# Kernel tuning notes

Hardware: AMD Instinct MI355X
Metric: run time of the kernel (lower is better)

The kernel has to match this reference:

```python
import jax, jax.numpy as jnp
import numpy as np

EPS = 1e-08

def rotate_half(x):
    # split last dim into 2 halves: '... (j d) -> ... j d', j=2
    x1, x2 = jnp.split(x, 2, axis=-1)
    return jnp.concatenate((-x2, x1), axis=-1)

def apply_rotary_pos_emb(t, freqs):
    seq_len = t.shape[-2]
    freqs = freqs[:, :, -seq_len:]
    return t * jnp.cos(freqs) + rotate_half(t) * jnp.sin(freqs)

def setup_inputs() -> dict:
    key = jax.random.key(0)
    ks = jax.random.split(key, 6)
    B, N, D, H, DH = 2, 2048, 1024, 16, 64
    inner = H * DH
    x = jax.random.normal(ks[0], (B, N, D), dtype=jnp.float32)
    # realistic rotary frequencies over dim_head
    inv_freq = 1.0 / (10000.0 ** (np.arange(0, DH, 2, dtype=np.float32) / DH))
    t = np.arange(N, dtype=np.float32)
    freqs = np.einsum('n,f->nf', t, inv_freq)            # [N, DH/2]
    pos_emb = jnp.asarray(np.concatenate([freqs, freqs], axis=-1)[None, None])  # [1,1,N,DH]
    gamma = jnp.ones((D,), dtype=jnp.float32)
    Wq = jax.random.normal(ks[1], (D, inner), dtype=jnp.float32) * (D ** -0.5)
    Wkv = jax.random.normal(ks[2], (D, 2 * inner), dtype=jnp.float32) * (D ** -0.5)
    Wo = jax.random.normal(ks[3], (inner, D), dtype=jnp.float32) * (inner ** -0.5)
    bo = jnp.zeros((D,), dtype=jnp.float32)
    return {"x": x, "pos_emb": pos_emb, "gamma": gamma, "Wq": Wq, "Wkv": Wkv, "Wo": Wo, "bo": bo}

def reference(x, pos_emb, gamma, Wq, Wkv, Wo, bo):
    B, N, D = x.shape
    H = 16
    DH = Wq.shape[1] // H
    scale = DH ** -0.5
    # NOTE: kv_input is the UN-normalized x (captured before RMSNorm in the original)
    kv_input = x
    # RMSNorm: x / clamp(||x|| * dim^-0.5, eps) * gamma
    norm = jnp.linalg.norm(x, axis=-1, keepdims=True) * (D ** -0.5)
    xn = x / jnp.maximum(norm, EPS) * gamma
    q = xn @ Wq                                   # [B,N,H*DH]
    kv = kv_input @ Wkv
    k, v = jnp.split(kv, 2, axis=-1)
    def to_heads(t):
        return t.reshape(B, N, H, DH).transpose(0, 2, 1, 3)  # b h n d
    q, k, v = to_heads(q), to_heads(k), to_heads(v)
    q = q * scale
    q = apply_rotary_pos_emb(q, pos_emb)
    k = apply_rotary_pos_emb(k, pos_emb)
    sim = jnp.einsum('bhid,bhjd->bhij', q, k)
    i, j = sim.shape[-2:]
    causal_mask = jnp.triu(jnp.ones((i, j), dtype=bool), k=j - i + 1)
    mask_value = -jnp.finfo(sim.dtype).max
    sim = jnp.where(causal_mask, mask_value, sim)
    attn = jax.nn.softmax(sim, axis=-1)
    out = jnp.einsum('bhij,bhjd->bhid', attn, v)
    out = out.transpose(0, 2, 1, 3).reshape(B, N, H * DH)
    return out @ Wo + bo
```

## Files before the change

### kernel.cpp

```cpp
#include <hip/hip_runtime.h>
#include <cmath>

#define B_ 2
#define N_ 2048
#define D_ 1024
#define H_ 16

typedef __attribute__((ext_vector_type(8))) short short8;
typedef __attribute__((ext_vector_type(4))) float f32x4;
typedef __attribute__((ext_vector_type(4))) unsigned short u16x4;

__device__ __forceinline__ unsigned short f2bf(float f) {
    union { float f; unsigned u; } x;
    x.f = f;
    unsigned r = x.u + 0x7FFFu + ((x.u >> 16) & 1u);
    return (unsigned short)(r >> 16);
}
__device__ __forceinline__ float bf2f(unsigned short u) {
    union { unsigned u; float f; } x;
    x.u = ((unsigned)u) << 16;
    return x.f;
}
__device__ __forceinline__ unsigned cvt_pk_bf16(float lo, float hi) {
    unsigned r;
    asm("v_cvt_pk_bf16_f32 %0, %1, %2" : "=v"(r) : "v"(lo), "v"(hi));
    return r;
}
__device__ __forceinline__ float exp2_fast(float x) {
    float r;
    asm("v_exp_f32 %0, %1" : "=v"(r) : "v"(x));
    return r;
}
__device__ __forceinline__ void gload_lds16(const void* g, void* l) {
    __builtin_amdgcn_global_load_lds((const __attribute__((address_space(1))) unsigned*)g,
                                     (__attribute__((address_space(3))) unsigned*)l,
                                     16, 0, 0);
}

__global__ __launch_bounds__(256) void freqtab_kernel(const float* __restrict__ pos,
                                                      float2* __restrict__ tabq,
                                                      float2* __restrict__ tabk) {
    const int idx = blockIdx.x * 256 + threadIdx.x;
    const float f = pos[idx];
    const float cc = cosf(f), ss = sinf(f);
    const float sq = 0.125f * 1.4426950408889634f;
    tabq[idx] = make_float2(sq * cc, sq * ss);
    tabk[idx] = make_float2(cc, ss);
}

__global__ __launch_bounds__(256) void rmsnorm_kernel(const float* __restrict__ x,
                                                      unsigned short* __restrict__ xb,
                                                      float* __restrict__ s) {
    const int row = blockIdx.x;
    const float4 v = reinterpret_cast<const float4*>(x + (size_t)row * D_)[threadIdx.x];
    float ss = v.x * v.x + v.y * v.y + v.z * v.z + v.w * v.w;
    #pragma unroll
    for (int off = 32; off; off >>= 1) ss += __shfl_xor(ss, off, 64);
    __shared__ float wss[4];
    if ((threadIdx.x & 63) == 0) wss[threadIdx.x >> 6] = ss;
    __syncthreads();
    const float tot = wss[0] + wss[1] + wss[2] + wss[3];
    const float inv = 1.0f / fmaxf(sqrtf(tot * (1.0f / D_)), 1e-8f);
    if (threadIdx.x == 0) s[row] = inv;
    u16x4 ox;
    ox[0] = f2bf(v.x); ox[1] = f2bf(v.y); ox[2] = f2bf(v.z); ox[3] = f2bf(v.w);
    *reinterpret_cast<u16x4*>(xb + (size_t)row * D_ + threadIdx.x * 4) = ox;
}

__global__ __launch_bounds__(256) void convT_all_kernel(const float* __restrict__ Wq,
                                                        const float* __restrict__ Wkv,
                                                        const float* __restrict__ Wo,
                                                        const float* __restrict__ gamma,
                                                        unsigned short* __restrict__ Wqt,
                                                        unsigned short* __restrict__ Wkvt,
                                                        unsigned short* __restrict__ Wot) {
    __shared__ float tile[32][33];
    const int bx = blockIdx.x;
    const float* W;
    unsigned short* Wt;
    int Nm, n0;
    bool gmul = false;
    if (bx < 32)       { W = Wq;  Wt = Wqt;  Nm = 1024; n0 = bx * 32; gmul = true; }
    else if (bx < 96)  { W = Wkv; Wt = Wkvt; Nm = 2048; n0 = (bx - 32) * 32; }
    else               { W = Wo;  Wt = Wot;  Nm = 1024; n0 = (bx - 96) * 32; }
    const int k0 = blockIdx.y * 32;
    const int r = threadIdx.x >> 3, c4 = (threadIdx.x & 7) * 4;
    const float4 ld = *reinterpret_cast<const float4*>(W + (size_t)(k0 + r) * Nm + n0 + c4);
    tile[r][c4 + 0] = ld.x; tile[r][c4 + 1] = ld.y;
    tile[r][c4 + 2] = ld.z; tile[r][c4 + 3] = ld.w;
    __syncthreads();
    u16x4 o;
    #pragma unroll
    for (int j = 0; j < 4; ++j) {
        float v = tile[c4 + j][r];
        if (gmul) v *= gamma[k0 + c4 + j];
        o[j] = f2bf(v);
    }
    *reinterpret_cast<u16x4*>(Wt + (size_t)(n0 + r) * 1024 + k0 + c4) = o;
}

__global__ __launch_bounds__(256) void gemm_qkv_kernel(const unsigned short* __restrict__ xb,
                                                       const unsigned short* __restrict__ Wqt,
                                                       const unsigned short* __restrict__ Wkvt,
                                                       const float* __restrict__ s,
                                                       unsigned short* __restrict__ qb,
                                                       unsigned short* __restrict__ kb,
                                                       unsigned short* __restrict__ vt,
                                                       const float2* __restrict__ tabq,
                                                       const float2* __restrict__ tabk) {
    __shared__ unsigned short As[2][64 * 64];
    __shared__ unsigned short Bs[2][128 * 64];
    __shared__ float sld[64];
    const int bid = blockIdx.x;
    const int xcd = bid & 7;
    const int ii = bid >> 3;
    const int bx = xcd * 3 + (ii % 3);
    const int m0 = (ii / 3) * 64;

    const unsigned short* Bt;
    int n0;
    if (bx < 8)       { Bt = Wqt;  n0 = bx * 128; }
    else if (bx < 16) { Bt = Wkvt; n0 = (bx - 8) * 128; }
    else              { Bt = Wkvt; n0 = (bx - 16) * 128 + 1024; }

    const int tid = threadIdx.x, lane = tid & 63, w = tid >> 6;
    const int wm = w >> 1, wn = w & 1;
    const int cc = lane & 15;
    const int sr = tid >> 3;
    const int sc = (tid & 7) * 8;

    if (tid < 64) sld[tid] = s[m0 + tid];

    f32x4 acc[2][4] = {};

    #pragma unroll
    for (int i = 0; i < 4; ++i) {
        const int r = i * 32 + sr;
        const int cs = sc ^ ((r & 7) << 3);
        if (i < 2)
            gload_lds16(xb + (size_t)(m0 + r) * 1024 + cs, (char*)As[0] + i * 4096 + w * 1024);
        gload_lds16(Bt + (size_t)(n0 + r) * 1024 + cs, (char*)Bs[0] + i * 4096 + w * 1024);
    }

    for (int t = 0; t < 16; ++t) {
        if (t + 1 < 16) {
            const int k0 = (t + 1) * 64;
            char* ad = (char*)As[(t + 1) & 1];
            char* bd = (char*)Bs[(t + 1) & 1];
            #pragma unroll
            for (int i = 0; i < 4; ++i) {
                const int r = i * 32 + sr;
                const int cs = sc ^ ((r & 7) << 3);
                if (i < 2)
                    gload_lds16(xb + (size_t)(m0 + r) * 1024 + k0 + cs, ad + i * 4096 + w * 1024);
                gload_lds16(Bt + (size_t)(n0 + r) * 1024 + k0 + cs, bd + i * 4096 + w * 1024);
            }
            asm volatile("s_waitcnt vmcnt(6)" ::: "memory");
        } else {
            asm volatile("s_waitcnt vmcnt(0)" ::: "memory");
        }
        __builtin_amdgcn_s_barrier();

        const char* Ac = (const char*)As[t & 1];
        const char* Bc = (const char*)Bs[t & 1];

        short8 af[2][2], bf[4][2];
        #pragma unroll
        for (int mf = 0; mf < 2; ++mf)
            #pragma unroll
            for (int ks = 0; ks < 2; ++ks) {
                const int r = wm * 32 + mf * 16 + cc;
                const int cb = (ks * 64 + ((lane >> 4) * 16)) ^ ((r & 7) << 4);
                af[mf][ks] = *reinterpret_cast<const short8*>(Ac + r * 128 + cb);
            }
        #pragma unroll
        for (int nf = 0; nf < 4; ++nf)
            #pragma unroll
            for (int ks = 0; ks < 2; ++ks) {
                const int r = wn * 64 + nf * 16 + cc;
                const int cb = (ks * 64 + ((lane >> 4) * 16)) ^ ((r & 7) << 4);
                bf[nf][ks] = *reinterpret_cast<const short8*>(Bc + r * 128 + cb);
            }
        #pragma unroll
        for (int ks = 0; ks < 2; ++ks)
            #pragma unroll
            for (int mf = 0; mf < 2; ++mf)
                #pragma unroll
                for (int nf = 0; nf < 4; ++nf)
                    acc[mf][nf] = __builtin_amdgcn_mfma_f32_16x16x32_bf16(af[mf][ks], bf[nf][ks], acc[mf][nf], 0, 0, 0);

        __builtin_amdgcn_s_barrier();
    }

    if (bx < 16) {
        const float2* tab = (bx < 8) ? tabq : tabk;
        unsigned short* dst = (bx < 8) ? qb : kb;
        const bool doscale = (bx < 8);
        #pragma unroll
        for (int mf = 0; mf < 2; ++mf)
            #pragma unroll
            for (int reg = 0; reg < 4; ++reg) {
                const int rloc = wm * 32 + mf * 16 + (lane >> 4) * 4 + reg;
                const int row = m0 + rloc;
                const int n = row & (N_ - 1);
                const float srow = doscale ? sld[rloc] : 1.0f;
                #pragma unroll
                for (int nf = 0; nf < 2; ++nf) {
                    const int d = nf * 16 + cc;
                    const float2 t1 = tab[n * 64 + d];
                    const float2 t2 = tab[n * 64 + 32 + d];
                    const float x1 = acc[mf][nf][reg] * srow;
                    const float x2 = acc[mf][nf + 2][reg] * srow;
                    const float o1 = x1 * t1.x - x2 * t1.y;
                    const float o2 = x2 * t2.x + x1 * t2.y;
                    const int col = n0 + wn * 64 + nf * 16 + cc;
                    dst[(size_t)row * 1024 + col] = f2bf(o1);
                    dst[(size_t)row * 1024 + col + 32] = f2bf(o2);
                }
            }
    } else {
        const int bb = m0 >> 11;
        const int nbase = (m0 & (N_ - 1)) + wm * 32;
        #pragma unroll
        for (int mf = 0; mf < 2; ++mf) {
            const int nloc = nbase + mf * 16 + (lane >> 4) * 4;
            #pragma unroll
            for (int nf = 0; nf < 4; ++nf) {
                const int cv = n0 - 1024 + wn * 64 + nf * 16 + cc;
                const int h = cv >> 6, d = cv & 63;
                uint2 u;
                u.x = cvt_pk_bf16(acc[mf][nf][0], acc[mf][nf][1]);
                u.y = cvt_pk_bf16(acc[mf][nf][2], acc[mf][nf][3]);
                *reinterpret_cast<uint2*>(vt + ((size_t)(bb * 16 + h) * 64 + d) * 2048 + nloc) = u;
            }
        }
    }
}

__global__ __launch_bounds__(256) void gemm_o_kernel(const unsigned short* __restrict__ A,
                                                     const unsigned short* __restrict__ Bt,
                                                     const float* __restrict__ bias,
                                                     float* __restrict__ Cout) {
    __shared__ unsigned short As[2][128 * 64];
    __shared__ unsigned short Bs[2][64 * 64];
    const int bid = blockIdx.x;
    const int xcd = bid & 7;
    const int ii = bid >> 3;
    const int n0 = (xcd * 2 + (ii & 1)) * 64;
    const int m0 = (ii >> 1) * 128;
    const int tid = threadIdx.x, lane = tid & 63, w = tid >> 6;
    const int wm = w >> 1, wn = w & 1;
    const int cc = lane & 15;
    const int sr = tid >> 3;
    const int sc = (tid & 7) * 8;

    f32x4 acc[4][2] = {};

    #pragma unroll
    for (int i = 0; i < 4; ++i) {
        const int r = i * 32 + sr;
        const int cs = sc ^ ((r & 7) << 3);
        gload_lds16(A + (size_t)(m0 + r) * 1024 + cs, (char*)As[0] + i * 4096 + w * 1024);
        if (i < 2)
            gload_lds16(Bt + (size_t)(n0 + r) * 1024 + cs, (char*)Bs[0] + i * 4096 + w * 1024);
    }

    for (int t = 0; t < 16; ++t) {
        if (t + 1 < 16) {
            const int k0 = (t + 1) * 64;
            char* ad = (char*)As[(t + 1) & 1];
            char* bd = (char*)Bs[(t + 1) & 1];
            #pragma unroll
            for (int i = 0; i < 4; ++i) {
                const int r = i * 32 + sr;
                const int cs = sc ^ ((r & 7) << 3);
                gload_lds16(A + (size_t)(m0 + r) * 1024 + k0 + cs, ad + i * 4096 + w * 1024);
                if (i < 2)
                    gload_lds16(Bt + (size_t)(n0 + r) * 1024 + k0 + cs, bd + i * 4096 + w * 1024);
            }
            asm volatile("s_waitcnt vmcnt(6)" ::: "memory");
        } else {
            asm volatile("s_waitcnt vmcnt(0)" ::: "memory");
        }
        __builtin_amdgcn_s_barrier();

        const char* Ac = (const char*)As[t & 1];
        const char* Bc = (const char*)Bs[t & 1];

        short8 af[4][2], bf[2][2];
        #pragma unroll
        for (int mf = 0; mf < 4; ++mf)
            #pragma unroll
            for (int ks = 0; ks < 2; ++ks) {
                const int r = wm * 64 + mf * 16 + cc;
                const int cb = (ks * 64 + ((lane >> 4) * 16)) ^ ((r & 7) << 4);
                af[mf][ks] = *reinterpret_cast<const short8*>(Ac + r * 128 + cb);
            }
        #pragma unroll
        for (int nf = 0; nf < 2; ++nf)
            #pragma unroll
            for (int ks = 0; ks < 2; ++ks) {
                const int r = wn * 32 + nf * 16 + cc;
                const int cb = (ks * 64 + ((lane >> 4) * 16)) ^ ((r & 7) << 4);
                bf[nf][ks] = *reinterpret_cast<const short8*>(Bc + r * 128 + cb);
            }
        #pragma unroll
        for (int ks = 0; ks < 2; ++ks)
            #pragma unroll
            for (int mf = 0; mf < 4; ++mf)
                #pragma unroll
                for (int nf = 0; nf < 2; ++nf)
                    acc[mf][nf] = __builtin_amdgcn_mfma_f32_16x16x32_bf16(af[mf][ks], bf[nf][ks], acc[mf][nf], 0, 0, 0);

        __builtin_amdgcn_s_barrier();
    }

    float bb[2];
    #pragma unroll
    for (int nf = 0; nf < 2; ++nf) bb[nf] = bias[n0 + wn * 32 + nf * 16 + cc];
    #pragma unroll
    for (int mf = 0; mf < 4; ++mf)
        #pragma unroll
        for (int nf = 0; nf < 2; ++nf)
            #pragma unroll
            for (int reg = 0; reg < 4; ++reg) {
                const int row = m0 + wm * 64 + mf * 16 + (lane >> 4) * 4 + reg;
                const int col = n0 + wn * 32 + nf * 16 + cc;
                Cout[(size_t)row * 1024 + col] = acc[mf][nf][reg] + bb[nf];
            }
}

__global__ __launch_bounds__(256, 5) void attn_mfma_kernel(const unsigned short* __restrict__ q,
                                                           const unsigned short* __restrict__ kb,
                                                           const unsigned short* __restrict__ vt,
                                                           unsigned short* __restrict__ att,
                                                           unsigned short* __restrict__ pO,
                                                           float2* __restrict__ pml) {
    const int bid = blockIdx.x;
    const int xcd = bid & 7;
    const int rest = bid >> 3;
    const int bh = xcd * 4 + rest / 48;
    const int s = 47 - (rest % 48);
    int qi, t0, t1, half;
    bool split;
    if (s < 16) {
        qi = s; t0 = 0; t1 = qi + 1; half = 0; split = false;
    } else {
        const int qs = s - 16;
        qi = 16 + (qs >> 1);
        half = qs & 1;
        const int hmid = (qi + 2) >> 1;
        t0 = half ? hmid : 0;
        t1 = half ? (qi + 1) : hmid;
        split = true;
    }
    const int b = bh >> 4, h = bh & 15;
    const int qb_ = qi * 64;
    const int tid = threadIdx.x;
    const int lane = tid & 63;
    const int w = tid >> 6;
    const int c = lane & 15;
    const int g = lane >> 4;

    __shared__ __align__(16) unsigned short Ks[2][64 * 64];
    __shared__ __align__(16) unsigned short Vs[64 * 64];
    __shared__ __align__(16) unsigned short Ps[4][1024];
    char* const PB = (char*)&Ps[w][0];

    const int qrow = qb_ + w * 16 + c;
    short8 qf[2];
    {
        const unsigned short* qp = q + (size_t)(b * N_ + qrow) * 1024 + h * 64 + g * 8;
        qf[0] = *reinterpret_cast<const short8*>(qp);
        qf[1] = *reinterpret_cast<const short8*>(qp + 32);
    }

    float m = -1e30f, l = 0.f;
    f32x4 oacc[4] = {};

    const int sr = tid >> 3, sc = (tid & 7) * 8;
    const unsigned short* kbase = kb + (size_t)b * N_ * 1024 + h * 64;
    const unsigned short* vbase = vt + (size_t)bh * 64 * 2048;

    #pragma unroll
    for (int i = 0; i < 2; ++i) {
        const int r = i * 32 + sr;
        const int cs = sc ^ ((r & 7) << 3);
        gload_lds16(kbase + (size_t)(t0 * 64 + r) * 1024 + cs,
                    (char*)Ks[t0 & 1] + i * 4096 + w * 1024);
        gload_lds16(vbase + (size_t)r * 2048 + t0 * 64 + cs,
                    (char*)Vs + i * 4096 + w * 1024);
    }

    for (int t = t0; t < t1; ++t) {
        const int jb = t * 64;
        const int jn = jb + 64;
        if (t + 1 < t1) {
            char* kd = (char*)Ks[(t + 1) & 1];
            #pragma unroll
            for (int i = 0; i < 2; ++i) {
                const int r = i * 32 + sr;
                const int cs = sc ^ ((r & 7) << 3);
                gload_lds16(kbase + (size_t)(jn + r) * 1024 + cs, kd + i * 4096 + w * 1024);
            }
            asm volatile("s_waitcnt vmcnt(2)" ::: "memory");
        } else {
            asm volatile("s_waitcnt vmcnt(0)" ::: "memory");
        }
        __builtin_amdgcn_s_barrier();

        const char* Ksc = (const char*)Ks[t & 1];
        const char* Vsc = (const char*)Vs;

        f32x4 st[4];
        __builtin_amdgcn_s_setprio(1);
        #pragma unroll
        for (int ct = 0; ct < 4; ++ct) {
            const int key = ct * 16 + c;
            f32x4 acc = {0.f, 0.f, 0.f, 0.f};
            #pragma unroll
            for (int ks = 0; ks < 2; ++ks) {
                const int addr = (key * 128 + ks * 64 + g * 16) ^ ((key & 7) << 4);
                const short8 kf = *reinterpret_cast<const short8*>(Ksc + addr);
                acc = __builtin_amdgcn_mfma_f32_16x16x32_bf16(kf, qf[ks], acc, 0, 0, 0);
            }
            st[ct] = acc;
        }
        __builtin_amdgcn_s_setprio(0);

        float mx = -1e30f;
        if (jb + 63 > qrow) {
            #pragma unroll
            for (int ct = 0; ct < 4; ++ct)
                #pragma unroll
                for (int reg = 0; reg < 4; ++reg) {
                    const int key = jb + ct * 16 + g * 4 + reg;
                    const float sv = (key <= qrow) ? st[ct][reg] : -1e30f;
                    st[ct][reg] = sv;
                    mx = fmaxf(mx, sv);
                }
        } else {
            #pragma unroll
            for (int ct = 0; ct < 4; ++ct)
                mx = fmaxf(mx, fmaxf(fmaxf(st[ct][0], st[ct][1]),
                                     fmaxf(st[ct][2], st[ct][3])));
        }
        mx = fmaxf(mx, __shfl_xor(mx, 16, 64));
        mx = fmaxf(mx, __shfl_xor(mx, 32, 64));
        if (!__all(mx <= m + 8.0f)) {
            const float mn = fmaxf(m, mx);
            const float corr = exp2_fast(m - mn);
            l *= corr;
            m = mn;
            #pragma unroll
            for (int dt = 0; dt < 4; ++dt) {
                oacc[dt][0] *= corr; oacc[dt][1] *= corr;
                oacc[dt][2] *= corr; oacc[dt][3] *= corr;
            }
        }
        float rs = 0.f;
        #pragma unroll
        for (int ct = 0; ct < 4; ++ct)
            #pragma unroll
            for (int reg = 0; reg < 4; ++reg) {
                const float p = exp2_fast(st[ct][reg] - m);
                st[ct][reg] = p;
                rs += p;
            }
        rs += __shfl_xor(rs, 16, 64);
        rs += __shfl_xor(rs, 32, 64);
        l += rs;

        #pragma unroll
        for (int ct = 0; ct < 4; ++ct) {
            uint2 u;
            u.x = cvt_pk_bf16(st[ct][0], st[ct][1]);
            u.y = cvt_pk_bf16(st[ct][2], st[ct][3]);
            const int addr = (c * 128 + ct * 32 + g * 8) ^ ((c & 7) << 4);
            *reinterpret_cast<uint2*>(PB + addr) = u;
        }
        short8 pf[2];
        #pragma unroll
        for (int ks = 0; ks < 2; ++ks) {
            const int addr = (c * 128 + ks * 64 + g * 16) ^ ((c & 7) << 4);
            pf[ks] = *reinterpret_cast<const short8*>(PB + addr);
        }
        __builtin_amdgcn_s_setprio(1);
        #pragma unroll
        for (int dt = 0; dt < 4; ++dt) {
            #pragma unroll
            for (int ks = 0; ks < 2; ++ks) {
                const int vd = dt * 16 + c;
                const int addr = (vd * 128 + ks * 64 + g * 16) ^ ((vd & 7) << 4);
                const short8 vf = *reinterpret_cast<const short8*>(Vsc + addr);
                oacc[dt] = __builtin_amdgcn_mfma_f32_16x16x32_bf16(vf, pf[ks], oacc[dt], 0, 0, 0);
            }
        }
        __builtin_amdgcn_s_setprio(0);

        __builtin_amdgcn_s_barrier();

        if (t + 1 < t1) {
            #pragma unroll
            for (int i = 0; i < 2; ++i) {
                const int r = i * 32 + sr;
                const int cs = sc ^ ((r & 7) << 3);
                gload_lds16(vbase + (size_t)r * 2048 + jn + cs, (char*)Vs + i * 4096 + w * 1024);
            }
        }
    }

    if (!split) {
        const float inv = 1.0f / l;
        unsigned short* orow = att + (size_t)(b * N_ + qrow) * 1024 + h * 64;
        #pragma unroll
        for (int dt = 0; dt < 4; ++dt) {
            #pragma unroll
            for (int rp = 0; rp < 2; ++rp) {
                const unsigned u = cvt_pk_bf16(oacc[dt][2 * rp] * inv,
                                               oacc[dt][2 * rp + 1] * inv);
                *reinterpret_cast<unsigned*>(orow + dt * 16 + g * 4 + rp * 2) = u;
            }
        }
    } else {
        const int slot = (bh * 16 + (qi - 16)) * 2 + half;
        const int rloc = w * 16 + c;
        pml[slot * 64 + rloc] = make_float2(m, l);
        unsigned short* prow = pO + (size_t)slot * 4096 + rloc * 64;
        #pragma unroll
        for (int dt = 0; dt < 4; ++dt) {
            #pragma unroll
            for (int rp = 0; rp < 2; ++rp) {
                const unsigned u = cvt_pk_bf16(oacc[dt][2 * rp], oacc[dt][2 * rp + 1]);
                *reinterpret_cast<unsigned*>(prow + dt * 16 + g * 4 + rp * 2) = u;
            }
        }
    }
}

__global__ __launch_bounds__(256) void attn_merge_kernel(const unsigned short* __restrict__ pO,
                                                         const float2* __restrict__ pml,
                                                         unsigned short* __restrict__ att) {
    const int blk = blockIdx.x;
    const int bh = blk >> 4;
    const int qt = blk & 15;
    const int qi = 16 + qt;
    const int b = bh >> 4, h = bh & 15;
    const int tid = threadIdx.x;
    const int row = tid >> 2;
    const int d0 = (tid & 3) * 16;
    const int slot0 = (bh * 16 + qt) * 2;
    const float2 ml0 = pml[slot0 * 64 + row];
    const float2 ml1 = pml[(slot0 + 1) * 64 + row];
    const float M = fmaxf(ml0.x, ml1.x);
    const float w0 = exp2_fast(ml0.x - M);
    const float w1 = exp2_fast(ml1.x - M);
    const float invL = 1.0f / (ml0.y * w0 + ml1.y * w1);
    const unsigned short* p0 = pO + (size_t)slot0 * 4096 + row * 64 + d0;
    const unsigned short* p1 = p0 + 4096;
    const int qrow = qi * 64 + row;
    unsigned short* orow = att + (size_t)(b * N_ + qrow) * 1024 + h * 64 + d0;
    #pragma unroll
    for (int j = 0; j < 16; j += 2) {
        const float a0 = (bf2f(p0[j]) * w0 + bf2f(p1[j]) * w1) * invL;
        const float a1 = (bf2f(p0[j + 1]) * w0 + bf2f(p1[j + 1]) * w1) * invL;
        *reinterpret_cast<unsigned*>(orow + j) = cvt_pk_bf16(a0, a1);
    }
}

extern "C" void kernel_launch(void* const* d_in, const int* in_sizes, int n_in,
                              void* d_out, int out_size, void* d_ws, size_t ws_size,
                              hipStream_t stream) {
    const float* x     = (const float*)d_in[0];
    const float* pos   = (const float*)d_in[1];
    const float* gamma = (const float*)d_in[2];
    const float* Wq    = (const float*)d_in[3];
    const float* Wkv   = (const float*)d_in[4];
    const float* Wo    = (const float*)d_in[5];
    const float* bo    = (const float*)d_in[6];
    float* out = (float*)d_out;
    char* ws = (char*)d_ws;

    const size_t MB = 1024 * 1024;
    unsigned short* kb   = (unsigned short*)(ws);
    unsigned short* qb   = (unsigned short*)(ws + 16 * MB);
    unsigned short* att  = (unsigned short*)(ws + 24 * MB);
    unsigned short* xb   = (unsigned short*)(ws + 32 * MB);
    unsigned short* Wqt  = (unsigned short*)(ws + 40 * MB);
    unsigned short* Wkvt = (unsigned short*)(ws + 42 * MB);
    unsigned short* Wot  = (unsigned short*)(ws + 46 * MB);
    unsigned short* vt   = (unsigned short*)(ws + 48 * MB);
    float2* tabq         = (float2*)(ws + 56 * MB);
    float2* tabk         = (float2*)(ws + 57 * MB);
    float* sv            = (float*)(ws + 58 * MB);
    unsigned short* pO   = (unsigned short*)(ws + 32 * MB);
    float2* pml          = (float2*)(ws + 40 * MB + 512 * 1024);

    freqtab_kernel<<<512, 256, 0, stream>>>(pos, tabq, tabk);
    convT_all_kernel<<<dim3(128, 32), 256, 0, stream>>>(Wq, Wkv, Wo, gamma, Wqt, Wkvt, Wot);
    rmsnorm_kernel<<<B_ * N_, 256, 0, stream>>>(x, xb, sv);

    gemm_qkv_kernel<<<1536, 256, 0, stream>>>(
        xb, Wqt, Wkvt, sv, qb, kb, vt, tabq, tabk);

    attn_mfma_kernel<<<1536, 256, 0, stream>>>(qb, kb, vt, att, pO, pml);
    attn_merge_kernel<<<512, 256, 0, stream>>>(pO, pml, att);

    gemm_o_kernel<<<512, 256, 0, stream>>>(att, Wot, bo, out);
}
```

Baseline: 120.2 us.

## Feed softmax probabilities to PV MFMA from registers via permuted V layout

Stops staging the bf16 probability tile through per-wave shared memory before the P·V MFMA and packs the registers straight into MFMA operands. To keep the sequence-to-k mapping consistent, the QKV GEMM epilogue now writes the transposed V tensor with its sequence positions permuted within each 32-row group. Dropping the P scratch buffer cuts LDS use, and the attention kernel's occupancy hint is raised from 5 to 6 blocks per CU. The risk is that the V permutation must match the register layout exactly, and the higher occupancy target tightens the register budget.

New measurement: 118.2 us (median of 2 runs). Within noise of the previous version (-1.7%).

```diff
diff --git a/kernel.cpp b/kernel.cpp
--- a/kernel.cpp
+++ b/kernel.cpp
@@ -9,6 +9,7 @@
 typedef __attribute__((ext_vector_type(8))) short short8;
 typedef __attribute__((ext_vector_type(4))) float f32x4;
 typedef __attribute__((ext_vector_type(4))) unsigned short u16x4;
+typedef __attribute__((ext_vector_type(4))) unsigned int uint4v;
 
 __device__ __forceinline__ unsigned short f2bf(float f) {
     union { float f; unsigned u; } x;
@@ -220,10 +221,11 @@
             }
     } else {
         const int bb = m0 >> 11;
-        const int nbase = (m0 & (N_ - 1)) + wm * 32;
+        const int gg = lane >> 4;
+        const int tb = m0 & (N_ - 1);
         #pragma unroll
         for (int mf = 0; mf < 2; ++mf) {
-            const int nloc = nbase + mf * 16 + (lane >> 4) * 4;
+            const int npos = tb + wm * 32 + (gg >> 1) * 16 + (gg & 1) * 8 + mf * 4;
             #pragma unroll
             for (int nf = 0; nf < 4; ++nf) {
                 const int cv = n0 - 1024 + wn * 64 + nf * 16 + cc;
@@ -231,7 +233,7 @@
                 uint2 u;
                 u.x = cvt_pk_bf16(acc[mf][nf][0], acc[mf][nf][1]);
                 u.y = cvt_pk_bf16(acc[mf][nf][2], acc[mf][nf][3]);
-                *reinterpret_cast<uint2*>(vt + ((size_t)(bb * 16 + h) * 64 + d) * 2048 + nloc) = u;
+                *reinterpret_cast<uint2*>(vt + ((size_t)(bb * 16 + h) * 64 + d) * 2048 + npos) = u;
             }
         }
     }
@@ -330,7 +332,7 @@
             }
 }
 
-__global__ __launch_bounds__(256, 5) void attn_mfma_kernel(const unsigned short* __restrict__ q,
+__global__ __launch_bounds__(256, 6) void attn_mfma_kernel(const unsigned short* __restrict__ q,
                                                            const unsigned short* __restrict__ kb,
                                                            const unsigned short* __restrict__ vt,
                                                            unsigned short* __restrict__ att,
@@ -364,8 +366,6 @@
 
     __shared__ __align__(16) unsigned short Ks[2][64 * 64];
     __shared__ __align__(16) unsigned short Vs[64 * 64];
-    __shared__ __align__(16) unsigned short Ps[4][1024];
-    char* const PB = (char*)&Ps[w][0];
 
     const int qrow = qb_ + w * 16 + c;
     short8 qf[2];
@@ -471,29 +471,31 @@
         rs += __shfl_xor(rs, 32, 64);
         l += rs;
 
-        #pragma unroll
-        for (int ct = 0; ct < 4; ++ct) {
-            uint2 u;
-            u.x = cvt_pk_bf16(st[ct][0], st[ct][1]);
-            u.y = cvt_pk_bf16(st[ct][2], st[ct][3]);
-            const int addr = (c * 128 + ct * 32 + g * 8) ^ ((c & 7) << 4);
-            *reinterpret_cast<uint2*>(PB + addr) = u;
-        }
-        short8 pf[2];
-        #pragma unroll
-        for (int ks = 0; ks < 2; ++ks) {
-            const int addr = (c * 128 + ks * 64 + g * 16) ^ ((c & 7) << 4);
-            pf[ks] = *reinterpret_cast<const short8*>(PB + addr);
-        }
+        uint4v pv0, pv1;
+        pv0[0] = cvt_pk_bf16(st[0][0], st[0][1]);
+        pv0[1] = cvt_pk_bf16(st[0][2], st[0][3]);
+        pv0[2] = cvt_pk_bf16(st[1][0], st[1][1]);
+        pv0[3] = cvt_pk_bf16(st[1][2], st[1][3]);
+        pv1[0] = cvt_pk_bf16(st[2][0], st[2][1]);
+        pv1[1] = cvt_pk_bf16(st[2][2], st[2][3]);
+        pv1[2] = cvt_pk_bf16(st[3][0], st[3][1]);
+        pv1[3] = cvt_pk_bf16(st[3][2], st[3][3]);
+        const short8 pf0 = *reinterpret_cast<const short8*>(&pv0);
+        const short8 pf1 = *reinterpret_cast<const short8*>(&pv1);
+
         __builtin_amdgcn_s_setprio(1);
         #pragma unroll
         for (int dt = 0; dt < 4; ++dt) {
-            #pragma unroll
-            for (int ks = 0; ks < 2; ++ks) {
-                const int vd = dt * 16 + c;
-                const int addr = (vd * 128 + ks * 64 + g * 16) ^ ((vd & 7) << 4);
+            const int vd = dt * 16 + c;
+            {
+                const int addr = (vd * 128 + 0 * 64 + g * 16) ^ ((vd & 7) << 4);
                 const short8 vf = *reinterpret_cast<const short8*>(Vsc + addr);
-                oacc[dt] = __builtin_amdgcn_mfma_f32_16x16x32_bf16(vf, pf[ks], oacc[dt], 0, 0, 0);
+                oacc[dt] = __builtin_amdgcn_mfma_f32_16x16x32_bf16(vf, pf0, oacc[dt], 0, 0, 0);
+            }
+            {
+                const int addr = (vd * 128 + 1 * 64 + g * 16) ^ ((vd & 7) << 4);
+                const short8 vf = *reinterpret_cast<const short8*>(Vsc + addr);
+                oacc[dt] = __builtin_amdgcn_mfma_f32_16x16x32_bf16(vf, pf1, oacc[dt], 0, 0, 0);
             }
         }
         __builtin_amdgcn_s_setprio(0);
```

## Process two query tiles per wave in attention and drop LDS P round-trip

Applied to the files above, without the earlier changes.

The attention kernel now runs 2 waves per block instead of 4, and each wave handles 32 query rows as two 16-row tiles. Each K fragment read from LDS is reused for two MFMAs, and the V fragment likewise, which halves LDS traffic per unit of compute. The P matrix stays in registers by permuting the V-transpose store layout in the QKV GEMM epilogue, so the LDS write/read shuffle for P is removed. This raises register pressure and cuts waves per block, which may hurt latency hiding.

Result: no change. 122.3 us (+1.7%).

```diff
diff --git a/kernel.cpp b/kernel.cpp
--- a/kernel.cpp
+++ b/kernel.cpp
@@ -9,6 +9,7 @@
 typedef __attribute__((ext_vector_type(8))) short short8;
 typedef __attribute__((ext_vector_type(4))) float f32x4;
 typedef __attribute__((ext_vector_type(4))) unsigned short u16x4;
+typedef __attribute__((ext_vector_type(4))) unsigned int uint4v;
 
 __device__ __forceinline__ unsigned short f2bf(float f) {
     union { float f; unsigned u; } x;
@@ -220,10 +221,11 @@
             }
     } else {
         const int bb = m0 >> 11;
-        const int nbase = (m0 & (N_ - 1)) + wm * 32;
+        const int gg = lane >> 4;
+        const int tb = m0 & (N_ - 1);
         #pragma unroll
         for (int mf = 0; mf < 2; ++mf) {
-            const int nloc = nbase + mf * 16 + (lane >> 4) * 4;
+            const int npos = tb + wm * 32 + (gg >> 1) * 16 + (gg & 1) * 8 + mf * 4;
             #pragma unroll
             for (int nf = 0; nf < 4; ++nf) {
                 const int cv = n0 - 1024 + wn * 64 + nf * 16 + cc;
@@ -231,7 +233,7 @@
                 uint2 u;
                 u.x = cvt_pk_bf16(acc[mf][nf][0], acc[mf][nf][1]);
                 u.y = cvt_pk_bf16(acc[mf][nf][2], acc[mf][nf][3]);
-                *reinterpret_cast<uint2*>(vt + ((size_t)(bb * 16 + h) * 64 + d) * 2048 + nloc) = u;
+                *reinterpret_cast<uint2*>(vt + ((size_t)(bb * 16 + h) * 64 + d) * 2048 + npos) = u;
             }
         }
     }
@@ -330,7 +332,7 @@
             }
 }
 
-__global__ __launch_bounds__(256, 5) void attn_mfma_kernel(const unsigned short* __restrict__ q,
+__global__ __launch_bounds__(128, 3) void attn_mfma_kernel(const unsigned short* __restrict__ q,
                                                            const unsigned short* __restrict__ kb,
                                                            const unsigned short* __restrict__ vt,
                                                            unsigned short* __restrict__ att,
@@ -364,32 +366,32 @@
 
     __shared__ __align__(16) unsigned short Ks[2][64 * 64];
     __shared__ __align__(16) unsigned short Vs[64 * 64];
-    __shared__ __align__(16) unsigned short Ps[4][1024];
-    char* const PB = (char*)&Ps[w][0];
-
-    const int qrow = qb_ + w * 16 + c;
-    short8 qf[2];
-    {
-        const unsigned short* qp = q + (size_t)(b * N_ + qrow) * 1024 + h * 64 + g * 8;
-        qf[0] = *reinterpret_cast<const short8*>(qp);
-        qf[1] = *reinterpret_cast<const short8*>(qp + 32);
-    }
-
-    float m = -1e30f, l = 0.f;
-    f32x4 oacc[4] = {};
+
+    short8 qf[2][2];
+    int qrow[2];
+    #pragma unroll
+    for (int qt = 0; qt < 2; ++qt) {
+        qrow[qt] = qb_ + w * 32 + qt * 16 + c;
+        const unsigned short* qp = q + (size_t)(b * N_ + qrow[qt]) * 1024 + h * 64 + g * 8;
+        qf[qt][0] = *reinterpret_cast<const short8*>(qp);
+        qf[qt][1] = *reinterpret_cast<const short8*>(qp + 32);
+    }
+
+    float m[2] = {-1e30f, -1e30f}, l[2] = {0.f, 0.f};
+    f32x4 oacc[2][4] = {};
 
     const int sr = tid >> 3, sc = (tid & 7) * 8;
     const unsigned short* kbase = kb + (size_t)b * N_ * 1024 + h * 64;
     const unsigned short* vbase = vt + (size_t)bh * 64 * 2048;
 
     #pragma unroll
-    for (int i = 0; i < 2; ++i) {
-        const int r = i * 32 + sr;
+    for (int i = 0; i < 4; ++i) {
+        const int r = i * 16 + sr;
         const int cs = sc ^ ((r & 7) << 3);
         gload_lds16(kbase + (size_t)(t0 * 64 + r) * 1024 + cs,
-                    (char*)Ks[t0 & 1] + i * 4096 + w * 1024);
+                    (char*)Ks[t0 & 1] + i * 2048 + w * 1024);
         gload_lds16(vbase + (size_t)r * 2048 + t0 * 64 + cs,
-                    (char*)Vs + i * 4096 + w * 1024);
+                    (char*)Vs + i * 2048 + w * 1024);
     }
 
     for (int t = t0; t < t1; ++t) {
@@ -398,12 +400,12 @@
         if (t + 1 < t1) {
             char* kd = (char*)Ks[(t + 1) & 1];
             #pragma unroll
-            for (int i = 0; i < 2; ++i) {
-                const int r = i * 32 + sr;
+            for (int i = 0; i < 4; ++i) {
+                const int r = i * 16 + sr;
                 const int cs = sc ^ ((r & 7) << 3);
-                gload_lds16(kbase + (size_t)(jn + r) * 1024 + cs, kd + i * 4096 + w * 1024);
-            }
-            asm volatile("s_waitcnt vmcnt(2)" ::: "memory");
+                gload_lds16(kbase + (size_t)(jn + r) * 1024 + cs, kd + i * 2048 + w * 1024);
+            }
+            asm volatile("s_waitcnt vmcnt(4)" ::: "memory");
         } else {
             asm volatile("s_waitcnt vmcnt(0)" ::: "memory");
         }
@@ -412,88 +414,99 @@
         const char* Ksc = (const char*)Ks[t & 1];
         const char* Vsc = (const char*)Vs;
 
-        f32x4 st[4];
+        f32x4 st[2][4];
+        #pragma unroll
+        for (int qt = 0; qt < 2; ++qt)
+            #pragma unroll
+            for (int ct = 0; ct < 4; ++ct) st[qt][ct] = f32x4{0.f, 0.f, 0.f, 0.f};
         __builtin_amdgcn_s_setprio(1);
         #pragma unroll
         for (int ct = 0; ct < 4; ++ct) {
             const int key = ct * 16 + c;
-            f32x4 acc = {0.f, 0.f, 0.f, 0.f};
             #pragma unroll
             for (int ks = 0; ks < 2; ++ks) {
                 const int addr = (key * 128 + ks * 64 + g * 16) ^ ((key & 7) << 4);
                 const short8 kf = *reinterpret_cast<const short8*>(Ksc + addr);
-                acc = __builtin_amdgcn_mfma_f32_16x16x32_bf16(kf, qf[ks], acc, 0, 0, 0);
-            }
-            st[ct] = acc;
+                st[0][ct] = __builtin_amdgcn_mfma_f32_16x16x32_bf16(kf, qf[0][ks], st[0][ct], 0, 0, 0);
+                st[1][ct] = __builtin_amdgcn_mfma_f32_16x16x32_bf16(kf, qf[1][ks], st[1][ct], 0, 0, 0);
+            }
         }
         __builtin_amdgcn_s_setprio(0);
 
-        float mx = -1e30f;
-        if (jb + 63 > qrow) {
+        short8 pf[2][2];
+        bool act[2];
+        #pragma unroll
+        for (int qt = 0; qt < 2; ++qt) {
+            act[qt] = (jb <= qb_ + w * 32 + qt * 16 + 15);
+            if (!act[qt]) continue;
+            float mx = -1e30f;
+            if (jb + 63 > qrow[qt]) {
+                #pragma unroll
+                for (int ct = 0; ct < 4; ++ct)
+                    #pragma unroll
+                    for (int reg = 0; reg < 4; ++reg) {
+                        const int key = jb + ct * 16 + g * 4 + reg;
+                        const float sv = (key <= qrow[qt]) ? st[qt][ct][reg] : -1e30f;
+                        st[qt][ct][reg] = sv;
+                        mx = fmaxf(mx, sv);
+                    }
+            } else {
+                #pragma unroll
+                for (int ct = 0; ct < 4; ++ct)
+                    mx = fmaxf(mx, fmaxf(fmaxf(st[qt][ct][0], st[qt][ct][1]),
+                                         fmaxf(st[qt][ct][2], st[qt][ct][3])));
+            }
+            mx = fmaxf(mx, __shfl_xor(mx, 16, 64));
+            mx = fmaxf(mx, __shfl_xor(mx, 32, 64));
+            if (!__all(mx <= m[qt] + 8.0f)) {
+                const float mn = fmaxf(m[qt], mx);
+                const float corr = exp2_fast(m[qt] - mn);
+                l[qt] *= corr;
+                m[qt] = mn;
+                #pragma unroll
+                for (int dt = 0; dt < 4; ++dt) {
+                    oacc[qt][dt][0] *= corr; oacc[qt][dt][1] *= corr;
+                    oacc[qt][dt][2] *= corr; oacc[qt][dt][3] *= corr;
+                }
+            }
+            float rs = 0.f;
             #pragma unroll
             for (int ct = 0; ct < 4; ++ct)
                 #pragma unroll
                 for (int reg = 0; reg < 4; ++reg) {
-                    const int key = jb + ct * 16 + g * 4 + reg;
-                    const float sv = (key <= qrow) ? st[ct][reg] : -1e30f;
-                    st[ct][reg] = sv;
-                    mx = fmaxf(mx, sv);
+                    const float p = exp2_fast(st[qt][ct][reg] - m[qt]);
+                    st[qt][ct][reg] = p;
+                    rs += p;
                 }
-        } else {
-            #pragma unroll
-            for (int ct = 0; ct < 4; ++ct)
-                mx = fmaxf(mx, fmaxf(fmaxf(st[ct][0], st[ct][1]),
-                                     fmaxf(st[ct][2], st[ct][3])));
-        }
-        mx = fmaxf(mx, __shfl_xor(mx, 16, 64));
-        mx = fmaxf(mx, __shfl_xor(mx, 32, 64));
-        if (!__all(mx <= m + 8.0f)) {
-            const float mn = fmaxf(m, mx);
-            const float corr = exp2_fast(m - mn);
-            l *= corr;
-            m = mn;
-            #pragma unroll
-            for (int dt = 0; dt < 4; ++dt) {
-                oacc[dt][0] *= corr; oacc[dt][1] *= corr;
-                oacc[dt][2] *= corr; oacc[dt][3] *= corr;
-            }
-        }
-        float rs = 0.f;
-        #pragma unroll
-        for (int ct = 0; ct < 4; ++ct)
-            #pragma unroll
-            for (int reg = 0; reg < 4; ++reg) {
-                const float p = exp2_fast(st[ct][reg] - m);
-                st[ct][reg] = p;
-                rs += p;
-            }
-        rs += __shfl_xor(rs, 16, 64);
-        rs += __shfl_xor(rs, 32, 64);
-        l += rs;
-
-        #pragma unroll
-        for (int ct = 0; ct < 4; ++ct) {
-            uint2 u;
-            u.x = cvt_pk_bf16(st[ct][0], st[ct][1]);
-            u.y = cvt_pk_bf16(st[ct][2], st[ct][3]);
-            const int addr = (c * 128 + ct * 32 + g * 8) ^ ((c & 7) << 4);
-            *reinterpret_cast<uint2*>(PB + addr) = u;
-        }
-        short8 pf[2];
-        #pragma unroll
-        for (int ks = 0; ks < 2; ++ks) {
-            const int addr = (c * 128 + ks * 64 + g * 16) ^ ((c & 7) << 4);
-            pf[ks] = *reinterpret_cast<const short8*>(PB + addr);
-        }
+            rs += __shfl_xor(rs, 16, 64);
+            rs += __shfl_xor(rs, 32, 64);
+            l[qt] += rs;
+
+            uint4v pv0, pv1;
+            pv0[0] = cvt_pk_bf16(st[qt][0][0], st[qt][0][1]);
+            pv0[1] = cvt_pk_bf16(st[qt][0][2], st[qt][0][3]);
+            pv0[2] = cvt_pk_bf16(st[qt][1][0], st[qt][1][1]);
+            pv0[3] = cvt_pk_bf16(st[qt][1][2], st[qt][1][3]);
+            pv1[0] = cvt_pk_bf16(st[qt][2][0], st[qt][2][1]);
+            pv1[1] = cvt_pk_bf16(st[qt][2][2], st[qt][2][3]);
+            pv1[2] = cvt_pk_bf16(st[qt][3][0], st[qt][3][1]);
+            pv1[3] = cvt_pk_bf16(st[qt][3][2], st[qt][3][3]);
+            pf[qt][0] = *reinterpret_cast<const short8*>(&pv0);
+            pf[qt][1] = *reinterpret_cast<const short8*>(&pv1);
+        }
+
         __builtin_amdgcn_s_setprio(1);
         #pragma unroll
         for (int dt = 0; dt < 4; ++dt) {
+            const int vd = dt * 16 + c;
             #pragma unroll
             for (int ks = 0; ks < 2; ++ks) {
-                const int vd = dt * 16 + c;
                 const int addr = (vd * 128 + ks * 64 + g * 16) ^ ((vd & 7) << 4);
                 const short8 vf = *reinterpret_cast<const short8*>(Vsc + addr);
-                oacc[dt] = __builtin_amdgcn_mfma_f32_16x16x32_bf16(vf, pf[ks], oacc[dt], 0, 0, 0);
+                if (act[0])
+                    oacc[0][dt] = __builtin_amdgcn_mfma_f32_16x16x32_bf16(vf, pf[0][ks], oacc[0][dt], 0, 0, 0);
+                if (act[1])
+                    oacc[1][dt] = __builtin_amdgcn_mfma_f32_16x16x32_bf16(vf, pf[1][ks], oacc[1][dt], 0, 0, 0);
             }
         }
         __builtin_amdgcn_s_setprio(0);
@@ -502,37 +515,40 @@
 
         if (t + 1 < t1) {
             #pragma unroll
-            for (int i = 0; i < 2; ++i) {
-                const int r = i * 32 + sr;
+            for (int i = 0; i < 4; ++i) {
+                const int r = i * 16 + sr;
                 const int cs = sc ^ ((r & 7) << 3);
-                gload_lds16(vbase + (size_t)r * 2048 + jn + cs, (char*)Vs + i * 4096 + w * 1024);
-            }
-        }
-    }
-
-    if (!split) {
-        const float inv = 1.0f / l;
-        unsigned short* orow = att + (size_t)(b * N_ + qrow) * 1024 + h * 64;
-        #pragma unroll
-        for (int dt = 0; dt < 4; ++dt) {
-            #pragma unroll
-            for (int rp = 0; rp < 2; ++rp) {
-                const unsigned u = cvt_pk_bf16(oacc[dt][2 * rp] * inv,
-                                               oacc[dt][2 * rp + 1] * inv);
-                *reinterpret_cast<unsigned*>(orow + dt * 16 + g * 4 + rp * 2) = u;
-            }
-        }
-    } else {
-        const int slot = (bh * 16 + (qi - 16)) * 2 + half;
-        const int rloc = w * 16 + c;
-        pml[slot * 64 + rloc] = make_float2(m, l);
-        unsigned short* prow = pO + (size_t)slot * 4096 + rloc * 64;
-        #pragma unroll
-        for (int dt = 0; dt < 4; ++dt) {
-            #pragma unroll
-            for (int rp = 0; rp < 2; ++rp) {
-                const unsigned u = cvt_pk_bf16(oacc[dt][2 * rp], oacc[dt][2 * rp + 1]);
-                *reinterpret_cast<unsigned*>(prow + dt * 16 + g * 4 + rp * 2) = u;
+                gload_lds16(vbase + (size_t)r * 2048 + jn + cs, (char*)Vs + i * 2048 + w * 1024);
+            }
+        }
+    }
+
+    #pragma unroll
+    for (int qt = 0; qt < 2; ++qt) {
+        if (!split) {
+            const float inv = 1.0f / l[qt];
+            unsigned short* orow = att + (size_t)(b * N_ + qrow[qt]) * 1024 + h * 64;
+            #pragma unroll
+            for (int dt = 0; dt < 4; ++dt) {
+                #pragma unroll
+                for (int rp = 0; rp < 2; ++rp) {
+                    const unsigned u = cvt_pk_bf16(oacc[qt][dt][2 * rp] * inv,
+                                                   oacc[qt][dt][2 * rp + 1] * inv);
+                    *reinterpret_cast<unsigned*>(orow + dt * 16 + g * 4 + rp * 2) = u;
+                }
+            }
+        } else {
+            const int slot = (bh * 16 + (qi - 16)) * 2 + half;
+            const int rloc = w * 32 + qt * 16 + c;
+            pml[slot * 64 + rloc] = make_float2(m[qt], l[qt]);
+            unsigned short* prow = pO + (size_t)slot * 4096 + rloc * 64;
+            #pragma unroll
+            for (int dt = 0; dt < 4; ++dt) {
+                #pragma unroll
+                for (int rp = 0; rp < 2; ++rp) {
+                    const unsigned u = cvt_pk_bf16(oacc[qt][dt][2 * rp], oacc[qt][dt][2 * rp + 1]);
+                    *reinterpret_cast<unsigned*>(prow + dt * 16 + g * 4 + rp * 2) = u;
+                }
             }
         }
     }
@@ -603,7 +619,7 @@
     gemm_qkv_kernel<<<1536, 256, 0, stream>>>(
         xb, Wqt, Wkvt, sv, qb, kb, vt, tabq, tabk);
 
-    attn_mfma_kernel<<<1536, 256, 0, stream>>>(qb, kb, vt, att, pO, pml);
+    attn_mfma_kernel<<<1536, 128, 0, stream>>>(qb, kb, vt, att, pO, pml);
     attn_merge_kernel<<<512, 256, 0, stream>>>(pO, pml, att);
 
     gemm_o_kernel<<<512, 256, 0, stream>>>(att, Wot, bo, out);
```
